# Kernel optimization log

Hardware: AMD Instinct MI355X
Metric: run time of the kernel (lower is better)

The kernel has to match this reference:

```python
import jax, jax.numpy as jnp
import numpy as np

# Standard 2D morphsnakes structuring elements (4 line filters), matching the
# repo-level global `filters` used by LSNet2.
_SE = np.zeros((4, 3, 3), dtype=np.float32)
_SE[0, 1, :] = 1.0           # horizontal line
_SE[1, :, 1] = 1.0           # vertical line
_SE[2] = np.eye(3, dtype=np.float32)          # main diagonal
_SE[3] = np.eye(3, dtype=np.float32)[::-1]    # anti-diagonal


def _dilate_stack(x, filts):
    # per-pixel: max over 3x3 window of (zero-padded x + filt), for every filter
    H, W = x.shape
    p = jnp.pad(x, 1)
    m = jnp.full((filts.shape[0], H, W), -jnp.inf, x.dtype)
    for k in range(3):
        for l in range(3):
            m = jnp.maximum(m, p[k:k + H, l:l + W][None] + filts[:, k, l][:, None, None])
    return m  # [F, H, W]


def _erode_stack(x, filts):
    # per-pixel: min over 3x3 window of (zero-padded x - filt) == -max(-(x - filt))
    H, W = x.shape
    p = jnp.pad(x, 1)
    m = jnp.full((filts.shape[0], H, W), jnp.inf, x.dtype)
    for k in range(3):
        for l in range(3):
            m = jnp.minimum(m, p[k:k + H, l:l + W][None] - filts[:, k, l][:, None, None])
    return m  # [F, H, W]


def _dilate_min(x, filts):
    return jnp.min(_dilate_stack(x, filts), axis=0)


def _erode_max(x, filts):
    return jnp.max(_erode_stack(x, filts), axis=0)


def setup_inputs() -> dict:
    key = jax.random.key(0)
    k1, k2 = jax.random.split(key)
    H = W = 2048
    inp = jax.random.uniform(k1, (H, W), dtype=jnp.float32)
    origin = jax.random.uniform(k2, (H, W), dtype=jnp.float32)
    filters = jnp.asarray(_SE)
    return {"input": inp, "origin": origin, "filters": filters}


def reference(input, origin, filters):
    x = input
    # SI o IS smoothing: dilate/min, erode/max, erode/max, dilate/min, dilate/min, erode/max
    x = _dilate_min(x, filters)
    x = _erode_max(x, filters)
    x = _erode_max(x, filters)
    x = _dilate_min(x, filters)
    x = _dilate_min(x, filters)
    x = _erode_max(x, filters)

    # balloon force with v = 1 and a flat ones(3,3) structuring element
    ones_f = jnp.ones((1, 3, 3), x.dtype)
    aux = _dilate_stack(x, ones_f)[0]
    threshold = jnp.percentile(x, 40.0)
    x = jnp.where(origin > threshold, aux, x)

    # Chan-Vese region means and update
    c0 = jnp.sum(origin * (1.0 - x)) / (jnp.sum(1.0 - x) + 1e-8)
    c1 = jnp.sum(origin * x) / (jnp.sum(x) + 1e-8)
    cv = (origin - c1) ** 2 - (origin - c0) ** 2
    x = jnp.where(cv < 0, 1.0, jnp.where(cv > 0, 0.0, x))
    return x
```

## Files before the change

### kernel.cpp

```cpp
#include <hip/hip_runtime.h>

#define HH 2048
#define WW 2048
#define NN (HH*WW)

static constexpr unsigned RANK0 = 1677721u;
static constexpr unsigned KEYLO = 0xB000u;
static constexpr unsigned KEYHI_ = 0xC000u;
static constexpr int NBINS = 4096;
static constexpr int NPART = 512;

#define TH 32
#define TW 128
#define LR 44
#define LCP 148

struct Scal {
  unsigned keyhiA, keyhiB, rA, rB;
  unsigned midA_, midB_, rA2, rB2;
  double thr, c0, c1;
};

static constexpr size_t OFF_CTL    = (size_t)NN * 4;
static constexpr size_t OFF_COARSE = OFF_CTL;
static constexpr size_t OFF_UNDER  = OFF_CTL + (size_t)NBINS * 4;
static constexpr size_t OFF_OVER   = OFF_UNDER + 4;
static constexpr size_t OFF_SCAL   = OFF_OVER + 4;
static constexpr size_t OFF_PART   = OFF_SCAL + 64;
static constexpr size_t OFF_MIDA   = OFF_PART + (size_t)NPART * 3 * 8;
static constexpr size_t OFF_MIDB   = OFF_MIDA + 1024;
static constexpr size_t OFF_LOWA   = OFF_MIDB + 1024;
static constexpr size_t OFF_LOWB   = OFF_LOWA + 1024;
static constexpr size_t WS_NEED    = OFF_LOWB + 1024;
static constexpr size_t CTL_BYTES  = WS_NEED - OFF_CTL;

__device__ __forceinline__ float mx3(float a, float b, float c){ return fmaxf(fmaxf(a,b),c); }
__device__ __forceinline__ float mn3(float a, float b, float c){ return fminf(fminf(a,b),c); }

__device__ __forceinline__ unsigned keyf(float x){
  unsigned b = __float_as_uint(x);
  return (b & 0x80000000u) ? ~b : (b | 0x80000000u);
}
__device__ __forceinline__ float keyinv(unsigned k){
  unsigned b = (k & 0x80000000u) ? (k ^ 0x80000000u) : ~k;
  return __uint_as_float(b);
}

__device__ __forceinline__ void loadrow(const float* __restrict__ src, int lr, int g, int lane,
                                        float4& v, float& L, float& R){
  v = *reinterpret_cast<const float4*>(&src[lr*LCP + 4*g]);
  L = __shfl_up(v.w, 1);
  R = __shfl_down(v.x, 1);
  if (lane == 0 || g == 0)   L = src[lr*LCP + (g ? 4*g - 1 : 0)];
  if (lane == 63 || g == 35) R = src[lr*LCP + ((g == 35) ? 143 : 4*g + 4)];
}

__device__ __forceinline__ void morph4(bool DIL,
    const float pr[6], const float cr[6], const float nr[6], float w[4]){
  #pragma unroll
  for (int i = 0; i < 4; i++){
    if (DIL){
      float Ah = mx3(cr[i],   cr[i+1], cr[i+2]);
      float Av = mx3(pr[i+1], cr[i+1], nr[i+1]);
      float Ad = mx3(pr[i],   cr[i+1], nr[i+2]);
      float Aa = mx3(pr[i+2], cr[i+1], nr[i]);
      float tm = mx3(pr[i], pr[i+1], pr[i+2]);
      float bm = mx3(nr[i], nr[i+1], nr[i+2]);
      float M9 = mx3(tm, Ah, bm);
      w[i] = fmaxf(M9, 1.0f + fminf(fminf(Ah,Av), fminf(Ad,Aa)));
    } else {
      float Bh = mn3(cr[i],   cr[i+1], cr[i+2]);
      float Bv = mn3(pr[i+1], cr[i+1], nr[i+1]);
      float Bd = mn3(pr[i],   cr[i+1], nr[i+2]);
      float Ba = mn3(pr[i+2], cr[i+1], nr[i]);
      float tm = mn3(pr[i], pr[i+1], pr[i+2]);
      float bm = mn3(nr[i], nr[i+1], nr[i+2]);
      float m9 = mn3(tm, Bh, bm);
      w[i] = fminf(m9, fmaxf(fmaxf(Bh,Bv), fmaxf(Bd,Ba)) - 1.0f);
    }
  }
}

__global__ __launch_bounds__(256)
void fused_morph_k(const float* __restrict__ in, float* __restrict__ out,
                   unsigned* __restrict__ gh, unsigned* __restrict__ under,
                   unsigned* __restrict__ over){
  __shared__ float lds[2][LR*LCP];
  const int tilec = blockIdx.x & 15;
  const int tiler = blockIdx.x >> 4;
  const int r0 = tiler*TH, c0 = tilec*TW;

  for (int idx = threadIdx.x; idx < LR*36; idx += 256){
    int lr = idx / 36, g = idx % 36;
    int gr = r0 - 6 + lr, gc = c0 - 8 + 4*g;
    float4 v = make_float4(0.f,0.f,0.f,0.f);
    if ((unsigned)gr < (unsigned)HH && (unsigned)gc < (unsigned)WW)
      v = *reinterpret_cast<const float4*>(in + (size_t)gr*WW + gc);
    *reinterpret_cast<float4*>(&lds[0][lr*LCP + 4*g]) = v;
  }
  __syncthreads();

  const int t = threadIdx.x;
  const int g = t % 36, s = t / 36;
  const bool active = (t < 252);
  const int lane = t & 63;
  const int gcBase = c0 - 8 + 4*g;
  const bool dilf[6] = {true,false,false,true,true,false};

  #pragma unroll 1
  for (int st = 0; st < 6; st++){
    const float* src = lds[st & 1];
    float*       dst = lds[(st & 1) ^ 1];
    if (active){
      const bool DIL = dilf[st];
      float4 vp, vc;  float pL,pR,cL,cR;
      loadrow(src, 6*s,     g, lane, vp, pL, pR);
      loadrow(src, 6*s + 1, g, lane, vc, cL, cR);
      #pragma unroll 1
      for (int k = 0; k < 6; k++){
        int lr = 6*s + 1 + k;
        float4 vn; float nL,nR;
        loadrow(src, lr + 1, g, lane, vn, nL, nR);
        float pr[6] = {pL, vp.x, vp.y, vp.z, vp.w, pR};
        float cr[6] = {cL, vc.x, vc.y, vc.z, vc.w, cR};
        float nr[6] = {nL, vn.x, vn.y, vn.z, vn.w, nR};
        float w[4];
        morph4(DIL, pr, cr, nr, w);
        int gr = r0 - 6 + lr;
        if ((unsigned)gr >= (unsigned)HH){
          w[0]=w[1]=w[2]=w[3]=0.f;
        } else {
          #pragma unroll
          for (int i = 0; i < 4; i++)
            if ((unsigned)(gcBase + i) >= (unsigned)WW) w[i] = 0.f;
        }
        *reinterpret_cast<float4*>(&dst[lr*LCP + 4*g]) = make_float4(w[0],w[1],w[2],w[3]);
        vp = vc; pL = cL; pR = cR;
        vc = vn; cL = nL; cR = nR;
      }
    }
    __syncthreads();
  }
  unsigned* lh = reinterpret_cast<unsigned*>(&lds[1][0]);
  for (int i = threadIdx.x; i < NBINS; i += 256) lh[i] = 0;
  __syncthreads();

  unsigned uc = 0, oc = 0;
  for (int idx = threadIdx.x; idx < TH*(TW/4); idx += 256){
    int row = idx >> 5, gg = idx & 31;
    float4 v = *reinterpret_cast<const float4*>(&lds[0][(row+6)*LCP + 8 + 4*gg]);
    *reinterpret_cast<float4*>(out + (size_t)(r0+row)*WW + c0 + 4*gg) = v;
    float vv[4] = {v.x, v.y, v.z, v.w};
    #pragma unroll
    for (int i = 0; i < 4; i++){
      unsigned key = keyf(vv[i]);
      unsigned hi = key >> 16;
      if (hi >= KEYLO && hi < KEYHI_) atomicAdd(&lh[hi - KEYLO], 1u);
      else if (hi < KEYLO)            uc++;
      else                            oc++;
    }
  }
  __syncthreads();
  for (int i = threadIdx.x; i < NBINS; i += 256){
    unsigned c = lh[i];
    if (c) atomicAdd(&gh[i], c);
  }
  if (uc) atomicAdd(under, uc);
  if (oc) atomicAdd(over, oc);
}

__global__ void scan_coarse_k(const unsigned* __restrict__ gh, const unsigned* __restrict__ under,
                              Scal* __restrict__ sc){
  __shared__ unsigned part[256];
  __shared__ unsigned excl[256];
  int t = threadIdx.x;
  unsigned loc = 0;
  #pragma unroll
  for (int i = 0; i < NBINS/256; i++) loc += gh[t*(NBINS/256) + i];
  part[t] = loc;
  __syncthreads();
  if (t == 0){
    unsigned run = under[0];
    for (int i = 0; i < 256; i++){ excl[i] = run; run += part[i]; }
  }
  __syncthreads();
  unsigned run = excl[t];
  const unsigned r0 = RANK0, r1 = RANK0 + 1;
  #pragma unroll
  for (int i = 0; i < NBINS/256; i++){
    unsigned idx = t*(NBINS/256) + i;
    unsigned cc = gh[idx];
    if (cc){
      if (r0 >= run && r0 - run < cc){ sc->keyhiA = KEYLO + idx; sc->rA = r0 - run; }
      if (r1 >= run && r1 - run < cc){ sc->keyhiB = KEYLO + idx; sc->rB = r1 - run; }
    }
    run += cc;
  }
}

__global__ __launch_bounds__(256)
void fine_mid_k(const float* __restrict__ x, const Scal* __restrict__ sc,
                unsigned* __restrict__ midA, unsigned* __restrict__ midB){
  __shared__ unsigned hA[256], hB[256];
  hA[threadIdx.x] = 0; hB[threadIdx.x] = 0;
  __syncthreads();
  unsigned ha = sc->keyhiA, hb = sc->keyhiB;
  bool dup = (ha == hb);
  const int nItems = NN/4;
  for (int it = blockIdx.x*blockDim.x + threadIdx.x; it < nItems; it += gridDim.x*blockDim.x){
    float4 v = reinterpret_cast<const float4*>(x)[it];
    float vv[4] = {v.x, v.y, v.z, v.w};
    #pragma unroll
    for (int t = 0; t < 4; t++){
      unsigned key = keyf(vv[t]);
      unsigned hi = key >> 16;
      if (hi == ha)      atomicAdd(&hA[(key >> 8) & 0xFFu], 1u);
      else if (hi == hb) atomicAdd(&hB[(key >> 8) & 0xFFu], 1u);
    }
  }
  __syncthreads();
  unsigned ca = hA[threadIdx.x];
  if (ca) atomicAdd(&midA[threadIdx.x], ca);
  if (!dup){
    unsigned cb = hB[threadIdx.x];
    if (cb) atomicAdd(&midB[threadIdx.x], cb);
  }
}

__global__ void scan_mid_k(const unsigned* __restrict__ midA, const unsigned* __restrict__ midB,
                           Scal* __restrict__ sc){
  __shared__ unsigned h[256], excl[256];
  int t = threadIdx.x;
  bool dup = (sc->keyhiA == sc->keyhiB);
  unsigned rA = sc->rA, rB = sc->rB;
  h[t] = midA[t];
  __syncthreads();
  if (t == 0){ unsigned run = 0; for (int i = 0; i < 256; i++){ excl[i] = run; run += h[i]; } }
  __syncthreads();
  if (rA >= excl[t] && rA - excl[t] < h[t]){ sc->midA_ = (unsigned)t; sc->rA2 = rA - excl[t]; }
  if (dup && rB >= excl[t] && rB - excl[t] < h[t]){ sc->midB_ = (unsigned)t; sc->rB2 = rB - excl[t]; }
  if (!dup){
    __syncthreads();
    h[t] = midB[t];
    __syncthreads();
    if (t == 0){ unsigned run = 0; for (int i = 0; i < 256; i++){ excl[i] = run; run += h[i]; } }
    __syncthreads();
    if (rB >= excl[t] && rB - excl[t] < h[t]){ sc->midB_ = (unsigned)t; sc->rB2 = rB - excl[t]; }
  }
}

__global__ __launch_bounds__(256)
void fine_low_k(const float* __restrict__ x, const Scal* __restrict__ sc,
                unsigned* __restrict__ lowA, unsigned* __restrict__ lowB){
  __shared__ unsigned hA[256], hB[256];
  hA[threadIdx.x] = 0; hB[threadIdx.x] = 0;
  __syncthreads();
  unsigned ha = sc->keyhiA, hb = sc->keyhiB;
  unsigned ma = sc->midA_, mb = sc->midB_;
  bool dup = (ha == hb) && (ma == mb);
  const int nItems = NN/4;
  for (int it = blockIdx.x*blockDim.x + threadIdx.x; it < nItems; it += gridDim.x*blockDim.x){
    float4 v = reinterpret_cast<const float4*>(x)[it];
    float vv[4] = {v.x, v.y, v.z, v.w};
    #pragma unroll
    for (int t = 0; t < 4; t++){
      unsigned key = keyf(vv[t]);
      unsigned hi = key >> 16;
      unsigned m  = (key >> 8) & 0xFFu;
      if (hi == ha && m == ma)      atomicAdd(&hA[key & 0xFFu], 1u);
      else if (hi == hb && m == mb) atomicAdd(&hB[key & 0xFFu], 1u);
    }
  }
  __syncthreads();
  unsigned ca = hA[threadIdx.x];
  if (ca) atomicAdd(&lowA[threadIdx.x], ca);
  if (!dup){
    unsigned cb = hB[threadIdx.x];
    if (cb) atomicAdd(&lowB[threadIdx.x], cb);
  }
}

__global__ void scan_low_k(const unsigned* __restrict__ lowA, const unsigned* __restrict__ lowB,
                           Scal* __restrict__ sc){
  __shared__ unsigned h[256], excl[256];
  __shared__ unsigned kfound[2];
  int t = threadIdx.x;
  bool dup = (sc->keyhiA == sc->keyhiB) && (sc->midA_ == sc->midB_);
  unsigned rA2 = sc->rA2, rB2 = sc->rB2;
  h[t] = lowA[t];
  __syncthreads();
  if (t == 0){ unsigned run = 0; for (int i = 0; i < 256; i++){ excl[i] = run; run += h[i]; } }
  __syncthreads();
  if (rA2 >= excl[t] && rA2 - excl[t] < h[t]) kfound[0] = (unsigned)t;
  if (dup && rB2 >= excl[t] && rB2 - excl[t] < h[t]) kfound[1] = (unsigned)t;
  if (!dup){
    __syncthreads();
    h[t] = lowB[t];
    __syncthreads();
    if (t == 0){ unsigned run = 0; for (int i = 0; i < 256; i++){ excl[i] = run; run += h[i]; } }
    __syncthreads();
    if (rB2 >= excl[t] && rB2 - excl[t] < h[t]) kfound[1] = (unsigned)t;
  }
  __syncthreads();
  if (t == 0){
    unsigned ka = (sc->keyhiA << 16) | (sc->midA_ << 8) | kfound[0];
    unsigned kb = (sc->keyhiB << 16) | (sc->midB_ << 8) | kfound[1];
    double va = (double)keyinv(ka), vb = (double)keyinv(kb);
    const double FRAC = 0.4*(double)(NN-1) - (double)RANK0;
    sc->thr = va + (vb - va) * FRAC;
  }
}

__device__ __forceinline__ void load6(const float* __restrict__ p, int row, int q, float r[6]){
  if (row < 0 || row >= HH){
    r[0]=r[1]=r[2]=r[3]=r[4]=r[5]=0.f;
    return;
  }
  const float* rp = p + (size_t)row * WW;
  float4 cc = *reinterpret_cast<const float4*>(rp + q);
  r[0] = (q > 0) ? rp[q-1] : 0.f;
  r[1]=cc.x; r[2]=cc.y; r[3]=cc.z; r[4]=cc.w;
  r[5] = (q+4 < WW) ? rp[q+4] : 0.f;
}

__global__ __launch_bounds__(256)
void balloon_k(const float* __restrict__ x, const float* __restrict__ orig,
               float* __restrict__ xb, const Scal* __restrict__ sc, double* __restrict__ part){
  double thr = sc->thr;
  double s0 = 0.0, s1 = 0.0, s2 = 0.0;
  const int nItems = NN/4;
  for (int it = blockIdx.x*blockDim.x + threadIdx.x; it < nItems; it += gridDim.x*blockDim.x){
    int i = it >> 9;
    int q = (it & 511) << 2;
    float a[6], b[6], c[6];
    load6(x, i-1, q, a);
    load6(x, i,   q, b);
    load6(x, i+1, q, c);
    float4 og = *reinterpret_cast<const float4*>(orig + (size_t)i*WW + q);
    float ov[4] = {og.x, og.y, og.z, og.w};
    float r[4];
    #pragma unroll
    for (int t = 0; t < 4; t++){
      float M9 = mx3(mx3(a[t],a[t+1],a[t+2]), mx3(b[t],b[t+1],b[t+2]), mx3(c[t],c[t+1],c[t+2]));
      float aux = 1.0f + M9;
      float nx = ((double)ov[t] > thr) ? aux : b[t+1];
      r[t] = nx;
      s0 += (double)ov[t];
      s1 += (double)nx;
      s2 += (double)ov[t] * (double)nx;
    }
    *reinterpret_cast<float4*>(xb + (size_t)i*WW + q) = make_float4(r[0],r[1],r[2],r[3]);
  }
  for (int off = 32; off > 0; off >>= 1){
    s0 += __shfl_down(s0, off);
    s1 += __shfl_down(s1, off);
    s2 += __shfl_down(s2, off);
  }
  __shared__ double red[4][3];
  int lane = threadIdx.x & 63, wv = threadIdx.x >> 6;
  if (lane == 0){ red[wv][0] = s0; red[wv][1] = s1; red[wv][2] = s2; }
  __syncthreads();
  if (threadIdx.x == 0){
    part[blockIdx.x*3+0] = red[0][0]+red[1][0]+red[2][0]+red[3][0];
    part[blockIdx.x*3+1] = red[0][1]+red[1][1]+red[2][1]+red[3][1];
    part[blockIdx.x*3+2] = red[0][2]+red[1][2]+red[2][2]+red[3][2];
  }
}

__global__ void c0c1_k(const double* __restrict__ part, Scal* __restrict__ sc){
  int t = threadIdx.x;
  double s0 = 0, s1 = 0, s2 = 0;
  for (int b = t; b < NPART; b += 256){
    s0 += part[b*3+0]; s1 += part[b*3+1]; s2 += part[b*3+2];
  }
  for (int off = 32; off > 0; off >>= 1){
    s0 += __shfl_down(s0, off);
    s1 += __shfl_down(s1, off);
    s2 += __shfl_down(s2, off);
  }
  __shared__ double red[4][3];
  int lane = t & 63, wv = t >> 6;
  if (lane == 0){ red[wv][0] = s0; red[wv][1] = s1; red[wv][2] = s2; }
  __syncthreads();
  if (t == 0){
    double So = red[0][0]+red[1][0]+red[2][0]+red[3][0];
    double Sx = red[0][1]+red[1][1]+red[2][1]+red[3][1];
    double Sox= red[0][2]+red[1][2]+red[2][2]+red[3][2];
    sc->c0 = (So - Sox) / ((double)NN - Sx + 1e-8);
    sc->c1 = Sox / (Sx + 1e-8);
  }
}

__global__ __launch_bounds__(256)
void final_k(const float* __restrict__ orig, const float* __restrict__ xb,
             const Scal* __restrict__ sc, float* __restrict__ out){
  double c0 = sc->c0, c1 = sc->c1;
  const int nItems = NN/4;
  for (int it = blockIdx.x*blockDim.x + threadIdx.x; it < nItems; it += gridDim.x*blockDim.x){
    float4 og = reinterpret_cast<const float4*>(orig)[it];
    float4 xv = reinterpret_cast<const float4*>(xb)[it];
    float ov[4] = {og.x, og.y, og.z, og.w};
    float xx[4] = {xv.x, xv.y, xv.z, xv.w};
    float r[4];
    #pragma unroll
    for (int t = 0; t < 4; t++){
      double o = (double)ov[t];
      double d1 = o - c1, d0 = o - c0;
      double cv = d1*d1 - d0*d0;
      r[t] = (cv < 0.0) ? 1.0f : ((cv > 0.0) ? 0.0f : xx[t]);
    }
    reinterpret_cast<float4*>(out)[it] = make_float4(r[0],r[1],r[2],r[3]);
  }
}

extern "C" void kernel_launch(void* const* d_in, const int* in_sizes, int n_in,
                              void* d_out, int out_size, void* d_ws, size_t ws_size,
                              hipStream_t stream) {
  const float* input  = (const float*)d_in[0];
  const float* origin = (const float*)d_in[1];
  float* out = (float*)d_out;

  char* ws = (char*)d_ws;
  float*    bufA   = (float*)ws;
  unsigned* coarse = (unsigned*)(ws + OFF_COARSE);
  unsigned* under  = (unsigned*)(ws + OFF_UNDER);
  unsigned* over   = (unsigned*)(ws + OFF_OVER);
  Scal*     scal   = (Scal*)(ws + OFF_SCAL);
  double*   part   = (double*)(ws + OFF_PART);
  unsigned* midA   = (unsigned*)(ws + OFF_MIDA);
  unsigned* midB   = (unsigned*)(ws + OFF_MIDB);
  unsigned* lowA   = (unsigned*)(ws + OFF_LOWA);
  unsigned* lowB   = (unsigned*)(ws + OFF_LOWB);

  hipMemsetAsync(ws + OFF_CTL, 0, CTL_BYTES, stream);

  fused_morph_k<<<(HH/TH)*(WW/TW), 256, 0, stream>>>(input, out, coarse, under, over);

  scan_coarse_k<<<1, 256, 0, stream>>>(coarse, under, scal);
  fine_mid_k<<<1024, 256, 0, stream>>>(out, scal, midA, midB);
  scan_mid_k<<<1, 256, 0, stream>>>(midA, midB, scal);
  fine_low_k<<<1024, 256, 0, stream>>>(out, scal, lowA, lowB);
  scan_low_k<<<1, 256, 0, stream>>>(lowA, lowB, scal);

  balloon_k<<<NPART, 256, 0, stream>>>(out, origin, bufA, scal, part);
  c0c1_k<<<1, 256, 0, stream>>>(part, scal);
  final_k<<<2048, 256, 0, stream>>>(origin, bufA, scal, out);
}
```

Measured before the change: 131.2 us.

## Merge mid and low radix-select passes into one pass with global 16-bit histogram

Replaces the two separate histogram passes over the morphed image (mid byte, then low byte) and their scan kernels with a single pass. That pass builds the mid-byte histogram in shared memory and a full 65536-bin low-16-bit histogram in global memory via global atomics. This removes one full 16 MB read and two kernel launches. In exchange it adds global atomics for elements in the selected coarse bucket and a larger memset of about 512 KB.

New measurement: 127.4 us. 1.03x faster.

```diff
diff --git a/kernel.cpp b/kernel.cpp
--- a/kernel.cpp
+++ b/kernel.cpp
@@ -17,22 +17,21 @@
 
 struct Scal {
   unsigned keyhiA, keyhiB, rA, rB;
-  unsigned midA_, midB_, rA2, rB2;
   double thr, c0, c1;
 };
 
 static constexpr size_t OFF_CTL    = (size_t)NN * 4;
 static constexpr size_t OFF_COARSE = OFF_CTL;
-static constexpr size_t OFF_UNDER  = OFF_CTL + (size_t)NBINS * 4;
+static constexpr size_t OFF_UNDER  = OFF_COARSE + (size_t)NBINS * 4;
 static constexpr size_t OFF_OVER   = OFF_UNDER + 4;
-static constexpr size_t OFF_SCAL   = OFF_OVER + 4;
+static constexpr size_t OFF_MIDA   = OFF_OVER + 4;
+static constexpr size_t OFF_MIDB   = OFF_MIDA + 1024;
+static constexpr size_t OFF_H2A    = OFF_MIDB + 1024;
+static constexpr size_t OFF_H2B    = OFF_H2A + 65536ull * 4;
+static constexpr size_t CTL_END    = OFF_H2B + 65536ull * 4;
+static constexpr size_t CTL_BYTES  = CTL_END - OFF_CTL;
+static constexpr size_t OFF_SCAL   = CTL_END;
 static constexpr size_t OFF_PART   = OFF_SCAL + 64;
-static constexpr size_t OFF_MIDA   = OFF_PART + (size_t)NPART * 3 * 8;
-static constexpr size_t OFF_MIDB   = OFF_MIDA + 1024;
-static constexpr size_t OFF_LOWA   = OFF_MIDB + 1024;
-static constexpr size_t OFF_LOWB   = OFF_LOWA + 1024;
-static constexpr size_t WS_NEED    = OFF_LOWB + 1024;
-static constexpr size_t CTL_BYTES  = WS_NEED - OFF_CTL;
 
 __device__ __forceinline__ float mx3(float a, float b, float c){ return fmaxf(fmaxf(a,b),c); }
 __device__ __forceinline__ float mn3(float a, float b, float c){ return fminf(fminf(a,b),c); }
@@ -199,8 +198,9 @@
 }
 
 __global__ __launch_bounds__(256)
-void fine_mid_k(const float* __restrict__ x, const Scal* __restrict__ sc,
-                unsigned* __restrict__ midA, unsigned* __restrict__ midB){
+void fine2d_k(const float* __restrict__ x, const Scal* __restrict__ sc,
+              unsigned* __restrict__ midA, unsigned* __restrict__ midB,
+              unsigned* __restrict__ h2A, unsigned* __restrict__ h2B){
   __shared__ unsigned hA[256], hB[256];
   hA[threadIdx.x] = 0; hB[threadIdx.x] = 0;
   __syncthreads();
@@ -211,100 +211,65 @@
     float4 v = reinterpret_cast<const float4*>(x)[it];
     float vv[4] = {v.x, v.y, v.z, v.w};
     #pragma unroll
-    for (int t = 0; t < 4; t++){
-      unsigned key = keyf(vv[t]);
+    for (int j = 0; j < 4; j++){
+      unsigned key = keyf(vv[j]);
       unsigned hi = key >> 16;
-      if (hi == ha)      atomicAdd(&hA[(key >> 8) & 0xFFu], 1u);
-      else if (hi == hb) atomicAdd(&hB[(key >> 8) & 0xFFu], 1u);
-    }
-  }
-  __syncthreads();
-  unsigned ca = hA[threadIdx.x];
-  if (ca) atomicAdd(&midA[threadIdx.x], ca);
-  if (!dup){
-    unsigned cb = hB[threadIdx.x];
-    if (cb) atomicAdd(&midB[threadIdx.x], cb);
-  }
-}
-
-__global__ void scan_mid_k(const unsigned* __restrict__ midA, const unsigned* __restrict__ midB,
-                           Scal* __restrict__ sc){
+      if (hi == ha){ atomicAdd(&hA[(key>>8)&255], 1u); atomicAdd(&h2A[key & 0xFFFFu], 1u); }
+      else if (hi == hb){ atomicAdd(&hB[(key>>8)&255], 1u); atomicAdd(&h2B[key & 0xFFFFu], 1u); }
+    }
+  }
+  __syncthreads();
+  if (hA[threadIdx.x]) atomicAdd(&midA[threadIdx.x], hA[threadIdx.x]);
+  if (!dup && hB[threadIdx.x]) atomicAdd(&midB[threadIdx.x], hB[threadIdx.x]);
+}
+
+__global__ void scan_ml_k(const unsigned* __restrict__ midA, const unsigned* __restrict__ midB,
+                          const unsigned* __restrict__ h2A, const unsigned* __restrict__ h2B,
+                          Scal* __restrict__ sc){
   __shared__ unsigned h[256], excl[256];
+  __shared__ unsigned res[6];
   int t = threadIdx.x;
-  bool dup = (sc->keyhiA == sc->keyhiB);
+  unsigned ha = sc->keyhiA, hb = sc->keyhiB;
+  bool dupHi = (ha == hb);
   unsigned rA = sc->rA, rB = sc->rB;
+
   h[t] = midA[t];
   __syncthreads();
   if (t == 0){ unsigned run = 0; for (int i = 0; i < 256; i++){ excl[i] = run; run += h[i]; } }
   __syncthreads();
-  if (rA >= excl[t] && rA - excl[t] < h[t]){ sc->midA_ = (unsigned)t; sc->rA2 = rA - excl[t]; }
-  if (dup && rB >= excl[t] && rB - excl[t] < h[t]){ sc->midB_ = (unsigned)t; sc->rB2 = rB - excl[t]; }
-  if (!dup){
-    __syncthreads();
+  if (rA >= excl[t] && rA - excl[t] < h[t]){ res[0] = (unsigned)t; res[1] = rA - excl[t]; }
+  if (dupHi && rB >= excl[t] && rB - excl[t] < h[t]){ res[2] = (unsigned)t; res[3] = rB - excl[t]; }
+  __syncthreads();
+  if (!dupHi){
     h[t] = midB[t];
     __syncthreads();
     if (t == 0){ unsigned run = 0; for (int i = 0; i < 256; i++){ excl[i] = run; run += h[i]; } }
     __syncthreads();
-    if (rB >= excl[t] && rB - excl[t] < h[t]){ sc->midB_ = (unsigned)t; sc->rB2 = rB - excl[t]; }
-  }
-}
-
-__global__ __launch_bounds__(256)
-void fine_low_k(const float* __restrict__ x, const Scal* __restrict__ sc,
-                unsigned* __restrict__ lowA, unsigned* __restrict__ lowB){
-  __shared__ unsigned hA[256], hB[256];
-  hA[threadIdx.x] = 0; hB[threadIdx.x] = 0;
-  __syncthreads();
-  unsigned ha = sc->keyhiA, hb = sc->keyhiB;
-  unsigned ma = sc->midA_, mb = sc->midB_;
-  bool dup = (ha == hb) && (ma == mb);
-  const int nItems = NN/4;
-  for (int it = blockIdx.x*blockDim.x + threadIdx.x; it < nItems; it += gridDim.x*blockDim.x){
-    float4 v = reinterpret_cast<const float4*>(x)[it];
-    float vv[4] = {v.x, v.y, v.z, v.w};
-    #pragma unroll
-    for (int t = 0; t < 4; t++){
-      unsigned key = keyf(vv[t]);
-      unsigned hi = key >> 16;
-      unsigned m  = (key >> 8) & 0xFFu;
-      if (hi == ha && m == ma)      atomicAdd(&hA[key & 0xFFu], 1u);
-      else if (hi == hb && m == mb) atomicAdd(&hB[key & 0xFFu], 1u);
-    }
-  }
-  __syncthreads();
-  unsigned ca = hA[threadIdx.x];
-  if (ca) atomicAdd(&lowA[threadIdx.x], ca);
-  if (!dup){
-    unsigned cb = hB[threadIdx.x];
-    if (cb) atomicAdd(&lowB[threadIdx.x], cb);
-  }
-}
-
-__global__ void scan_low_k(const unsigned* __restrict__ lowA, const unsigned* __restrict__ lowB,
-                           Scal* __restrict__ sc){
-  __shared__ unsigned h[256], excl[256];
-  __shared__ unsigned kfound[2];
-  int t = threadIdx.x;
-  bool dup = (sc->keyhiA == sc->keyhiB) && (sc->midA_ == sc->midB_);
-  unsigned rA2 = sc->rA2, rB2 = sc->rB2;
-  h[t] = lowA[t];
+    if (rB >= excl[t] && rB - excl[t] < h[t]){ res[2] = (unsigned)t; res[3] = rB - excl[t]; }
+    __syncthreads();
+  }
+  unsigned mA = res[0], rA2 = res[1], mB = res[2], rB2 = res[3];
+  bool dupMid = dupHi && (mA == mB);
+
+  h[t] = h2A[mA*256 + t];
   __syncthreads();
   if (t == 0){ unsigned run = 0; for (int i = 0; i < 256; i++){ excl[i] = run; run += h[i]; } }
   __syncthreads();
-  if (rA2 >= excl[t] && rA2 - excl[t] < h[t]) kfound[0] = (unsigned)t;
-  if (dup && rB2 >= excl[t] && rB2 - excl[t] < h[t]) kfound[1] = (unsigned)t;
-  if (!dup){
-    __syncthreads();
-    h[t] = lowB[t];
+  if (rA2 >= excl[t] && rA2 - excl[t] < h[t]) res[4] = (unsigned)t;
+  if (dupMid && rB2 >= excl[t] && rB2 - excl[t] < h[t]) res[5] = (unsigned)t;
+  __syncthreads();
+  if (!dupMid){
+    const unsigned* srcH = dupHi ? h2A : h2B;
+    h[t] = srcH[mB*256 + t];
     __syncthreads();
     if (t == 0){ unsigned run = 0; for (int i = 0; i < 256; i++){ excl[i] = run; run += h[i]; } }
     __syncthreads();
-    if (rB2 >= excl[t] && rB2 - excl[t] < h[t]) kfound[1] = (unsigned)t;
-  }
-  __syncthreads();
+    if (rB2 >= excl[t] && rB2 - excl[t] < h[t]) res[5] = (unsigned)t;
+    __syncthreads();
+  }
   if (t == 0){
-    unsigned ka = (sc->keyhiA << 16) | (sc->midA_ << 8) | kfound[0];
-    unsigned kb = (sc->keyhiB << 16) | (sc->midB_ << 8) | kfound[1];
+    unsigned ka = (ha << 16) | (mA << 8) | res[4];
+    unsigned kb = (hb << 16) | (mB << 8) | res[5];
     double va = (double)keyinv(ka), vb = (double)keyinv(kb);
     const double FRAC = 0.4*(double)(NN-1) - (double)RANK0;
     sc->thr = va + (vb - va) * FRAC;
@@ -425,22 +390,20 @@
   unsigned* coarse = (unsigned*)(ws + OFF_COARSE);
   unsigned* under  = (unsigned*)(ws + OFF_UNDER);
   unsigned* over   = (unsigned*)(ws + OFF_OVER);
+  unsigned* midA   = (unsigned*)(ws + OFF_MIDA);
+  unsigned* midB   = (unsigned*)(ws + OFF_MIDB);
+  unsigned* h2A    = (unsigned*)(ws + OFF_H2A);
+  unsigned* h2B    = (unsigned*)(ws + OFF_H2B);
   Scal*     scal   = (Scal*)(ws + OFF_SCAL);
   double*   part   = (double*)(ws + OFF_PART);
-  unsigned* midA   = (unsigned*)(ws + OFF_MIDA);
-  unsigned* midB   = (unsigned*)(ws + OFF_MIDB);
-  unsigned* lowA   = (unsigned*)(ws + OFF_LOWA);
-  unsigned* lowB   = (unsigned*)(ws + OFF_LOWB);
 
   hipMemsetAsync(ws + OFF_CTL, 0, CTL_BYTES, stream);
 
   fused_morph_k<<<(HH/TH)*(WW/TW), 256, 0, stream>>>(input, out, coarse, under, over);
 
   scan_coarse_k<<<1, 256, 0, stream>>>(coarse, under, scal);
-  fine_mid_k<<<1024, 256, 0, stream>>>(out, scal, midA, midB);
-  scan_mid_k<<<1, 256, 0, stream>>>(midA, midB, scal);
-  fine_low_k<<<1024, 256, 0, stream>>>(out, scal, lowA, lowB);
-  scan_low_k<<<1, 256, 0, stream>>>(lowA, lowB, scal);
+  fine2d_k<<<1024, 256, 0, stream>>>(out, scal, midA, midB, h2A, h2B);
+  scan_ml_k<<<1, 256, 0, stream>>>(midA, midB, h2A, h2B, scal);
 
   balloon_k<<<NPART, 256, 0, stream>>>(out, origin, bufA, scal, part);
   c0c1_k<<<1, 256, 0, stream>>>(part, scal);
```
